# Kernel tuning notes

Measured on AMD Instinct MI355X. Metric: run time of the kernel, lower is better.

The kernel has to match this reference:

```python
import jax, jax.numpy as jnp
import numpy as np
from jax import lax

B, T, N, HID = 4, 144, 256, 64
CH, NC = 9, 4  # chunk_size_short, num_chunks_short


def setup_inputs():
    key = jax.random.key(0)
    ks = jax.random.split(key, 30)
    r = lambda i, sh, s=0.05: jax.random.normal(ks[i], sh, jnp.float32) * s
    adj = (jax.random.uniform(ks[1], (N, N)) < 0.1).astype(jnp.float32)
    adj = adj.at[jnp.arange(N), jnp.arange(N)].set(1.0)  # self-loops
    return {
        "seg": jax.random.normal(ks[0], (B, T, N, N), jnp.float32),
        "adj": adj,
        "dist": jax.random.uniform(ks[2], (N, N), jnp.float32),
        "W_gat": r(3, (N, HID)),
        "a_src": r(4, (HID,)),
        "a_dst": r(5, (HID,)),
        "lstm_Wih": r(6, (4 * HID, HID)),
        "lstm_Whh": r(7, (4 * HID, HID)),
        "lstm_bih": r(8, (4 * HID,)),
        "lstm_bhh": r(9, (4 * HID,)),
        "attnL_W": r(10, (HID, HID)),
        "attnL_b": r(11, (HID,)),
        "attnL_v": r(12, (HID,)),
        "gru_Wih": r(13, (NC, 3 * HID, HID)),
        "gru_Whh": r(14, (NC, 3 * HID, HID)),
        "gru_bih": r(15, (NC, 3 * HID)),
        "gru_bhh": r(16, (NC, 3 * HID)),
        "attnS_W": r(17, (NC, HID, HID)),
        "attnS_b": r(18, (NC, HID)),
        "attnS_v": r(19, (NC, HID)),
        "lin1_W": r(20, (2 * HID, HID + HID * NC)),
        "lin1_b": r(21, (2 * HID,)),
        "lin2_W": r(22, (N * N, 2 * HID)),
        "lin2_b": r(23, (N * N,)),
        "conv_k": r(24, (1, 1, 3, 3)),
        "conv_b": r(25, (1,)),
    }


def gat_features(seg, adj, dist, W_gat, a_src, a_dst):
    # Batches the per-timestep GAT over the time axis (B,T folded together).
    Wh = jnp.einsum('btnf,fh->btnh', seg, W_gat)                     # (B,T,N,H)
    e = jax.nn.leaky_relu((Wh @ a_src)[..., :, None] + (Wh @ a_dst)[..., None, :], 0.2)
    e = e - dist                                                     # distance penalty on logits
    logits = jnp.where(adj > 0, e, -1e9)                             # mask non-edges
    attn = jax.nn.softmax(logits, axis=-1)                           # (B,T,N,N)
    Hn = jax.nn.elu(jnp.einsum('btij,btjh->btih', attn, Wh))         # (B,T,N,H)
    return Hn.mean(axis=2)                                           # (B,T,H) mean-pool over nodes


def lstm(x, Wih, Whh, bih, bhh):
    h0 = jnp.zeros((x.shape[0], Whh.shape[1]), x.dtype)
    def step(carry, xt):
        h, c = carry
        g = xt @ Wih.T + bih + h @ Whh.T + bhh
        i, f, gg, o = jnp.split(g, 4, axis=-1)  # torch gate order i,f,g,o
        c = jax.nn.sigmoid(f) * c + jax.nn.sigmoid(i) * jnp.tanh(gg)
        h = jax.nn.sigmoid(o) * jnp.tanh(c)
        return (h, c), h
    _, ys = lax.scan(step, (h0, h0), jnp.swapaxes(x, 0, 1))
    return jnp.swapaxes(ys, 0, 1)


def gru(x, Wih, Whh, bih, bhh):
    h0 = jnp.zeros((x.shape[0], Whh.shape[1]), x.dtype)
    def step(h, xt):
        gx = xt @ Wih.T + bih
        gh = h @ Whh.T + bhh
        xr, xz, xn = jnp.split(gx, 3, axis=-1)  # torch gate order r,z,n
        hr, hz, hn = jnp.split(gh, 3, axis=-1)
        rr = jax.nn.sigmoid(xr + hr)
        zz = jax.nn.sigmoid(xz + hz)
        nn_ = jnp.tanh(xn + rr * hn)
        h = (1.0 - zz) * nn_ + zz * h
        return h, h
    _, ys = lax.scan(step, h0, jnp.swapaxes(x, 0, 1))
    return jnp.swapaxes(ys, 0, 1)


def tattn(h, W, b, v):
    s = jnp.tanh(h @ W + b) @ v          # (B,T) additive attention scores
    a = jax.nn.softmax(s, axis=1)
    return jnp.einsum('bt,bth->bh', a, h)


def reference(seg, adj, dist, W_gat, a_src, a_dst, lstm_Wih, lstm_Whh, lstm_bih, lstm_bhh,
              attnL_W, attnL_b, attnL_v, gru_Wih, gru_Whh, gru_bih, gru_bhh,
              attnS_W, attnS_b, attnS_v, lin1_W, lin1_b, lin2_W, lin2_b, conv_k, conv_b):
    Bsz = seg.shape[0]
    feats = gat_features(seg, adj, dist, W_gat, a_src, a_dst)        # (B,T,H)
    ctxL = tattn(lstm(feats, lstm_Wih, lstm_Whh, lstm_bih, lstm_bhh), attnL_W, attnL_b, attnL_v)
    # Short-term GCN features are the same GAT outputs on the last W_short steps.
    short = feats[:, -CH * NC:, :].reshape(Bsz, NC, CH, HID)
    gru_out = jax.vmap(gru, in_axes=(1, 0, 0, 0, 0), out_axes=1)(short, gru_Wih, gru_Whh, gru_bih, gru_bhh)
    ctxS = jax.vmap(tattn, in_axes=(1, 0, 0, 0), out_axes=1)(gru_out, attnS_W, attnS_b, attnS_v)  # (B,NC,H)
    fused = jnp.concatenate([ctxL, ctxS.reshape(Bsz, NC * HID)], axis=1)  # (B, 5H)
    h1 = jax.nn.relu(fused @ lin1_W.T + lin1_b)
    out = (h1 @ lin2_W.T + lin2_b).reshape(Bsz, 1, N, N)
    out = lax.conv_general_dilated(out, conv_k, (1, 1), 'SAME',
                                   dimension_numbers=('NCHW', 'OIHW', 'NCHW'))
    out = out + conv_b[None, :, None, None]
    return jax.nn.softplus(out[:, 0])
```

## Files before the change

### kernel.cpp

```cpp
#include <hip/hip_runtime.h>
#include <hip/hip_bf16.h>
#include <cstddef>


typedef __attribute__((ext_vector_type(8))) short bf16x8;
typedef __attribute__((ext_vector_type(4))) short bf16x4;
typedef __attribute__((ext_vector_type(4))) float f32x4;

__device__ __forceinline__ float sigf(float x) { return 1.0f / (1.0f + __expf(-x)); }
__device__ __forceinline__ float tanh_(float x) {
    x = fminf(fmaxf(x, -15.f), 15.f);
    float e = __expf(2.f * x);
    return (e - 1.f) / (e + 1.f);
}
__device__ __forceinline__ unsigned short f2b(float f) {
    unsigned u = __float_as_uint(f);
    u += 0x7FFFu + ((u >> 16) & 1u);
    return (unsigned short)(u >> 16);
}

__global__ void k_prep(const float* __restrict__ adj, const float* __restrict__ dist,
                       const float* __restrict__ W_gat,
                       float* __restrict__ M, unsigned short* __restrict__ Wt) {
    int blk = blockIdx.x, tid = threadIdx.x;
    if (blk < 256) {
        int i = blk * 256 + tid;
        M[i] = (adj[i] > 0.f) ? -dist[i] : -1e9f;
    } else {
        for (int it = 0; it < 64; ++it) {
            int e = it * 256 + tid;
            int k = e >> 6, c = e & 63;
            Wt[c * 256 + k] = f2b(W_gat[e]);
        }
    }
}

__global__ __launch_bounds__(256, 2) void k_gat(
    const float* __restrict__ seg, const unsigned short* __restrict__ Wt,
    const float* __restrict__ a_src, const float* __restrict__ a_dst,
    const float* __restrict__ Mmask, float* __restrict__ feats,
    const float* __restrict__ lWih, const float* __restrict__ lbih,
    const float* __restrict__ lbhh, float* __restrict__ gx) {
    __shared__ __align__(16) short A_s[256 * 64];
    __shared__ __align__(16) short Wt_s[64 * 64];
    __shared__ __align__(16) short WhT_s[64 * 256];
    __shared__ __align__(16) float svec[256];
    __shared__ __align__(16) float dvec[256];
    __shared__ __align__(16) float rmax[256];
    __shared__ __align__(16) float red[256];
    __shared__ __align__(16) float feats_l[64];

    const int tid  = threadIdx.x;
    const int lane = tid & 63;
    const int wv   = tid >> 6;
    const int wrow = wv * 64;
    const int bt   = blockIdx.x;
    const float* __restrict__ segp = seg + (size_t)bt * 65536;

    f32x4 acc[4][4];
    #pragma unroll
    for (int a = 0; a < 4; ++a)
        #pragma unroll
        for (int b = 0; b < 4; ++b) acc[a][b] = (f32x4)(0.f);

    for (int kc = 0; kc < 4; ++kc) {
        #pragma unroll
        for (int it = 0; it < 8; ++it) {
            int unit = it * 256 + tid;
            int row = unit >> 3, u = unit & 7;
            const float* g = segp + row * 256 + kc * 64 + u * 8;
            f32x4 v0 = *(const f32x4*)g;
            f32x4 v1 = *(const f32x4*)(g + 4);
            bf16x8 pk;
            pk[0] = (short)f2b(v0[0]); pk[1] = (short)f2b(v0[1]);
            pk[2] = (short)f2b(v0[2]); pk[3] = (short)f2b(v0[3]);
            pk[4] = (short)f2b(v1[0]); pk[5] = (short)f2b(v1[1]);
            pk[6] = (short)f2b(v1[2]); pk[7] = (short)f2b(v1[3]);
            *(bf16x8*)&A_s[(row * 8 + (u ^ (row & 7))) * 8] = pk;
        }
        #pragma unroll
        for (int it = 0; it < 2; ++it) {
            int unit = it * 256 + tid;
            int c = unit >> 3, u = unit & 7;
            bf16x8 w = *(const bf16x8*)(Wt + c * 256 + kc * 64 + u * 8);
            *(bf16x8*)&Wt_s[(c * 8 + (u ^ (c & 7))) * 8] = w;
        }
        __syncthreads();
        #pragma unroll
        for (int kt2 = 0; kt2 < 2; ++kt2) {
            int ku = kt2 * 4 + (lane >> 4);
            bf16x8 bfr[4];
            #pragma unroll
            for (int nt = 0; nt < 4; ++nt) {
                int col = nt * 16 + (lane & 15);
                bfr[nt] = *(const bf16x8*)&Wt_s[(col * 8 + (ku ^ (col & 7))) * 8];
            }
            #pragma unroll
            for (int mt = 0; mt < 4; ++mt) {
                int row = wrow + mt * 16 + (lane & 15);
                bf16x8 afr = *(const bf16x8*)&A_s[(row * 8 + (ku ^ (row & 7))) * 8];
                #pragma unroll
                for (int nt = 0; nt < 4; ++nt)
                    acc[mt][nt] = __builtin_amdgcn_mfma_f32_16x16x32_bf16(afr, bfr[nt], acc[mt][nt], 0, 0, 0);
            }
        }
        __syncthreads();
    }

    float asv[4], adv[4];
    #pragma unroll
    for (int nt = 0; nt < 4; ++nt) {
        asv[nt] = a_src[nt * 16 + (lane & 15)];
        adv[nt] = a_dst[nt * 16 + (lane & 15)];
    }
    #pragma unroll
    for (int mt = 0; mt < 4; ++mt) {
        #pragma unroll
        for (int r = 0; r < 4; ++r) {
            float ps = acc[mt][0][r] * asv[0] + acc[mt][1][r] * asv[1]
                     + acc[mt][2][r] * asv[2] + acc[mt][3][r] * asv[3];
            float pd = acc[mt][0][r] * adv[0] + acc[mt][1][r] * adv[1]
                     + acc[mt][2][r] * adv[2] + acc[mt][3][r] * adv[3];
            #pragma unroll
            for (int m = 1; m < 16; m <<= 1) {
                ps += __shfl_xor(ps, m);
                pd += __shfl_xor(pd, m);
            }
            if ((lane & 15) == 0) {
                int row = wrow + mt * 16 + (lane >> 4) * 4 + r;
                svec[row] = ps;
                dvec[row] = pd;
            }
        }
        #pragma unroll
        for (int nt = 0; nt < 4; ++nt) {
            int col  = nt * 16 + (lane & 15);
            int row0 = wrow + mt * 16 + (lane >> 4) * 4;
            bf16x4 pk4;
            pk4[0] = (short)f2b(acc[mt][nt][0]); pk4[1] = (short)f2b(acc[mt][nt][1]);
            pk4[2] = (short)f2b(acc[mt][nt][2]); pk4[3] = (short)f2b(acc[mt][nt][3]);
            int addr16 = col * 32 + ((row0 >> 3) ^ (col & 7));
            *(bf16x4*)&WhT_s[addr16 * 8 + (row0 & 7)] = pk4;
        }
    }
    __syncthreads();

    {
        float s_i = svec[tid];
        float m = -3.0e38f;
        const float* Mrow = Mmask + tid * 256;
        #pragma unroll 4
        for (int j4 = 0; j4 < 64; ++j4) {
            f32x4 mv = *(const f32x4*)(Mrow + j4 * 4);
            f32x4 dv = *(const f32x4*)&dvec[j4 * 4];
            #pragma unroll
            for (int e = 0; e < 4; ++e) {
                float x = s_i + dv[e];
                x = (x > 0.f) ? x : 0.2f * x;
                x += mv[e];
                m = fmaxf(m, x);
            }
        }
        rmax[tid] = m;
    }
    __syncthreads();

    f32x4 acc2[4][4];
    #pragma unroll
    for (int a = 0; a < 4; ++a)
        #pragma unroll
        for (int b = 0; b < 4; ++b) acc2[a][b] = (f32x4)(0.f);
    float psum[4] = {0.f, 0.f, 0.f, 0.f};
    float sv4[4], mx4[4];
    #pragma unroll
    for (int mt = 0; mt < 4; ++mt) {
        int row = wrow + mt * 16 + (lane & 15);
        sv4[mt] = svec[row];
        mx4[mt] = rmax[row];
    }
    const int jbase = (lane >> 4) * 8;
    #pragma unroll 1
    for (int kt = 0; kt < 8; ++kt) {
        int j0 = kt * 32 + jbase;
        int ku = kt * 4 + (lane >> 4);
        bf16x8 bfr[4];
        #pragma unroll
        for (int nt = 0; nt < 4; ++nt) {
            int col = nt * 16 + (lane & 15);
            bfr[nt] = *(const bf16x8*)&WhT_s[(col * 32 + (ku ^ (col & 7))) * 8];
        }
        f32x4 dv0 = *(const f32x4*)&dvec[j0];
        f32x4 dv1 = *(const f32x4*)&dvec[j0 + 4];
        #pragma unroll
        for (int mt = 0; mt < 4; ++mt) {
            int row = wrow + mt * 16 + (lane & 15);
            const float* Mp = Mmask + row * 256 + j0;
            f32x4 m0 = *(const f32x4*)Mp;
            f32x4 m1 = *(const f32x4*)(Mp + 4);
            float p[8];
            #pragma unroll
            for (int e = 0; e < 4; ++e) {
                float x = sv4[mt] + dv0[e];
                x = (x > 0.f) ? x : 0.2f * x;
                p[e] = __expf(x + m0[e] - mx4[mt]);
                float y = sv4[mt] + dv1[e];
                y = (y > 0.f) ? y : 0.2f * y;
                p[4 + e] = __expf(y + m1[e] - mx4[mt]);
            }
            psum[mt] += ((p[0] + p[1]) + (p[2] + p[3])) + ((p[4] + p[5]) + (p[6] + p[7]));
            bf16x8 pf;
            pf[0] = (short)f2b(p[0]); pf[1] = (short)f2b(p[1]);
            pf[2] = (short)f2b(p[2]); pf[3] = (short)f2b(p[3]);
            pf[4] = (short)f2b(p[4]); pf[5] = (short)f2b(p[5]);
            pf[6] = (short)f2b(p[6]); pf[7] = (short)f2b(p[7]);
            #pragma unroll
            for (int nt = 0; nt < 4; ++nt)
                acc2[mt][nt] = __builtin_amdgcn_mfma_f32_16x16x32_bf16(pf, bfr[nt], acc2[mt][nt], 0, 0, 0);
        }
    }
    #pragma unroll
    for (int mt = 0; mt < 4; ++mt) {
        psum[mt] += __shfl_xor(psum[mt], 16);
        psum[mt] += __shfl_xor(psum[mt], 32);
    }

    float part[4] = {0.f, 0.f, 0.f, 0.f};
    #pragma unroll
    for (int mt = 0; mt < 4; ++mt) {
        #pragma unroll
        for (int r = 0; r < 4; ++r) {
            float rs  = __shfl(psum[mt], ((lane >> 4) << 2) + r);
            float inv = 1.0f / rs;
            #pragma unroll
            for (int nt = 0; nt < 4; ++nt) {
                float x = acc2[mt][nt][r] * inv;
                x = (x > 0.f) ? x : expm1f(x);
                part[nt] += x;
            }
        }
    }
    #pragma unroll
    for (int nt = 0; nt < 4; ++nt) {
        part[nt] += __shfl_xor(part[nt], 16);
        part[nt] += __shfl_xor(part[nt], 32);
    }
    if ((lane >> 4) == 0) {
        #pragma unroll
        for (int nt = 0; nt < 4; ++nt) red[wv * 64 + nt * 16 + lane] = part[nt];
    }
    __syncthreads();
    if (tid < 64) {
        float f = (red[tid] + red[64 + tid] + red[128 + tid] + red[192 + tid]) * (1.0f / 256.0f);
        feats[bt * 64 + tid] = f;
        feats_l[tid] = f;
    }
    __syncthreads();

    {
        float a = lbih[tid] + lbhh[tid];
        const float* wp = lWih + tid * 64;
        #pragma unroll
        for (int k4 = 0; k4 < 16; ++k4) {
            f32x4 w = *(const f32x4*)(wp + k4 * 4);
            f32x4 x = *(const f32x4*)&feats_l[k4 * 4];
            a += w[0] * x[0] + w[1] * x[1] + w[2] * x[2] + w[3] * x[3];
        }
        gx[bt * 256 + tid] = a;
    }
}

__global__ __launch_bounds__(256) void k_rnn(
    const float* __restrict__ gx, const float* __restrict__ lWhh, float* __restrict__ lout,
    const float* __restrict__ feats, const float* __restrict__ gWih,
    const float* __restrict__ gWhh, const float* __restrict__ gbih,
    const float* __restrict__ gbhh, float* __restrict__ gout) {
    int tid = threadIdx.x;
    if (blockIdx.x < 4) {
        int b = blockIdx.x;
        int lane = tid & 63, wv = tid >> 6;
        __shared__ __align__(16) float hv[4][64];
        __shared__ __align__(16) float gl[2][256];
        float wr[64];
        #pragma unroll
        for (int q = 0; q < 16; ++q)
            *(f32x4*)&wr[q * 4] = *(const f32x4*)&lWhh[tid * 64 + q * 4];
        float c_s = 0.f;
        hv[wv][lane] = 0.f;
        for (int t = 0; t < 144; ++t) {
            float a = gx[(b * 144 + t) * 256 + tid];
            #pragma unroll
            for (int q = 0; q < 16; ++q) {
                f32x4 h4 = *(const f32x4*)&hv[wv][q * 4];
                a += wr[q * 4 + 0] * h4[0] + wr[q * 4 + 1] * h4[1]
                   + wr[q * 4 + 2] * h4[2] + wr[q * 4 + 3] * h4[3];
            }
            gl[t & 1][tid] = a;
            __syncthreads();
            float ig = gl[t & 1][lane],       fg = gl[t & 1][64 + lane],
                  gg = gl[t & 1][128 + lane], og = gl[t & 1][192 + lane];
            c_s = sigf(fg) * c_s + sigf(ig) * tanh_(gg);
            float h = sigf(og) * tanh_(c_s);
            hv[wv][lane] = h;
            if (wv == 0) lout[(b * 144 + t) * 64 + lane] = h;
        }
    } else {
        int bi_ = blockIdx.x - 4;
        int b = bi_ >> 2, c2 = bi_ & 3;
        __shared__ float hvg[64], xvg[64], gxl[192], ghl[192];
        float wi[64], wh[64], bi = 0.f, bh = 0.f, h_s = 0.f;
        if (tid < 192) {
            #pragma unroll
            for (int q = 0; q < 16; ++q) {
                *(f32x4*)&wi[q * 4] = *(const f32x4*)&gWih[(size_t)(c2 * 192 + tid) * 64 + q * 4];
                *(f32x4*)&wh[q * 4] = *(const f32x4*)&gWhh[(size_t)(c2 * 192 + tid) * 64 + q * 4];
            }
            bi = gbih[c2 * 192 + tid];
            bh = gbhh[c2 * 192 + tid];
        }
        if (tid < 64) hvg[tid] = 0.f;
        __syncthreads();
        for (int s = 0; s < 9; ++s) {
            int t = 108 + c2 * 9 + s;
            if (tid < 64) xvg[tid] = feats[(b * 144 + t) * 64 + tid];
            __syncthreads();
            if (tid < 192) {
                float ax = bi, ah = bh;
                #pragma unroll
                for (int k = 0; k < 64; ++k) { ax += wi[k] * xvg[k]; ah += wh[k] * hvg[k]; }
                gxl[tid] = ax; ghl[tid] = ah;
            }
            __syncthreads();
            if (tid < 64) {
                float xr = gxl[tid], xz = gxl[64 + tid], xn = gxl[128 + tid];
                float hr = ghl[tid], hz = ghl[64 + tid], hn = ghl[128 + tid];
                float rr = sigf(xr + hr), zz = sigf(xz + hz);
                float nn = tanh_(xn + rr * hn);
                h_s = (1.f - zz) * nn + zz * h_s;
                hvg[tid] = h_s;
                gout[((b * 4 + c2) * 9 + s) * 64 + tid] = h_s;
            }
            __syncthreads();
        }
    }
}

__global__ __launch_bounds__(256) void k_ctx(
    const float* __restrict__ lout, const float* __restrict__ aLW,
    const float* __restrict__ aLb, const float* __restrict__ aLv,
    const float* __restrict__ gout, const float* __restrict__ aSW,
    const float* __restrict__ aSb, const float* __restrict__ aSv,
    float* __restrict__ ctxL, float* __restrict__ ctxS) {
    int tid = threadIdx.x;
    if (blockIdx.x < 4) {
        int b = blockIdx.x;
        int tt = tid >> 6, hh = tid & 63;
        __shared__ __align__(16) float hbuf[4][64];
        __shared__ float sc[144];
        __shared__ float al[144];
        float wcol[64];
        #pragma unroll
        for (int k = 0; k < 64; ++k) wcol[k] = aLW[k * 64 + hh];
        float bb = aLb[hh], vv = aLv[hh];
        for (int g = 0; g < 36; ++g) {
            int t = g * 4 + tt;
            hbuf[tt][hh] = lout[(b * 144 + t) * 64 + hh];
            __syncthreads();
            float acc = bb;
            #pragma unroll
            for (int q = 0; q < 16; ++q) {
                f32x4 h4 = *(const f32x4*)&hbuf[tt][q * 4];
                acc += wcol[q * 4 + 0] * h4[0] + wcol[q * 4 + 1] * h4[1]
                     + wcol[q * 4 + 2] * h4[2] + wcol[q * 4 + 3] * h4[3];
            }
            float p = tanh_(acc) * vv;
            #pragma unroll
            for (int m = 1; m < 64; m <<= 1) p += __shfl_xor(p, m);
            if (hh == 0) sc[t] = p;
            __syncthreads();
        }
        float mx = -3e38f;
        for (int t2 = 0; t2 < 144; ++t2) mx = fmaxf(mx, sc[t2]);
        float ss = 0.f;
        for (int t2 = 0; t2 < 144; ++t2) ss += __expf(sc[t2] - mx);
        float inv = 1.f / ss;
        if (tid < 144) al[tid] = __expf(sc[tid] - mx) * inv;
        __syncthreads();
        if (tid < 64) {
            float acc = 0.f;
            for (int t2 = 0; t2 < 144; ++t2) acc += al[t2] * lout[(b * 144 + t2) * 64 + tid];
            ctxL[b * 64 + tid] = acc;
        }
    } else {
        int bi_ = blockIdx.x - 4;
        int b = bi_ >> 2, c2 = bi_ & 3;
        __shared__ float xv2[64];
        if (tid < 64) {
            int lane = tid;
            const float* Wc = aSW + c2 * 4096;
            float wcol[64];
            #pragma unroll
            for (int k = 0; k < 64; ++k) wcol[k] = Wc[k * 64 + lane];
            float bb = aSb[c2 * 64 + lane], vv = aSv[c2 * 64 + lane];
            float sv[9], hl[9];
            #pragma unroll 1
            for (int s = 0; s < 9; ++s) {
                float h = gout[((size_t)((b * 4 + c2) * 9 + s)) * 64 + lane];
                hl[s] = h;
                xv2[lane] = h;
                float acc = bb;
                #pragma unroll
                for (int k = 0; k < 64; ++k) acc += wcol[k] * xv2[k];
                float p = tanh_(acc) * vv;
                #pragma unroll
                for (int m = 1; m < 64; m <<= 1) p += __shfl_xor(p, m);
                sv[s] = p;
            }
            float mx = -3e38f;
            #pragma unroll
            for (int s = 0; s < 9; ++s) mx = fmaxf(mx, sv[s]);
            float ss = 0.f;
            #pragma unroll
            for (int s = 0; s < 9; ++s) { sv[s] = __expf(sv[s] - mx); ss += sv[s]; }
            float inv = 1.f / ss;
            float acc = 0.f;
            #pragma unroll
            for (int s = 0; s < 9; ++s) acc += sv[s] * inv * hl[s];
            ctxS[(b * 4 + c2) * 64 + lane] = acc;
        }
    }
}

__global__ __launch_bounds__(512) void k_lin1(
    const float* __restrict__ ctxL, const float* __restrict__ ctxS,
    const float* __restrict__ W, const float* __restrict__ bb,
    float* __restrict__ h1) {
    int tid = threadIdx.x;
    __shared__ __align__(16) float fu[4 * 320];
    for (int c = tid; c < 1280; c += 512) {
        int b2 = c / 320, k = c % 320;
        fu[c] = (k < 64) ? ctxL[b2 * 64 + k] : ctxS[b2 * 256 + (k - 64)];
    }
    __syncthreads();
    int b = tid >> 7, r = tid & 127;
    float acc = bb[r];
    #pragma unroll 4
    for (int k4 = 0; k4 < 80; ++k4) {
        f32x4 w = *(const f32x4*)&W[r * 320 + k4 * 4];
        f32x4 x = *(const f32x4*)&fu[b * 320 + k4 * 4];
        acc += w[0] * x[0] + w[1] * x[1] + w[2] * x[2] + w[3] * x[3];
    }
    h1[b * 128 + r] = fmaxf(acc, 0.f);
}

__global__ __launch_bounds__(256) void k_lin2(
    const float* __restrict__ h1, const float* __restrict__ W,
    const float* __restrict__ bb, float* __restrict__ h2) {
    int tid = threadIdx.x, blk = blockIdx.x;
    __shared__ __align__(16) float Wc[256 * 33];
    __shared__ __align__(16) float h1l[512];
    for (int c = tid; c < 512; c += 256) h1l[c] = h1[c];
    int r = blk * 256 + tid;
    float a0, a1, a2, a3;
    a0 = a1 = a2 = a3 = bb[r];
    for (int kc = 0; kc < 4; ++kc) {
        __syncthreads();
        for (int it = 0; it < 32; ++it) {
            int c = it * 256 + tid;
            int row = c >> 5, kk = c & 31;
            Wc[row * 33 + kk] = W[(size_t)(blk * 256 + row) * 128 + kc * 32 + kk];
        }
        __syncthreads();
        #pragma unroll
        for (int kk = 0; kk < 32; ++kk) {
            float w = Wc[tid * 33 + kk];
            a0 += w * h1l[kc * 32 + kk];
            a1 += w * h1l[128 + kc * 32 + kk];
            a2 += w * h1l[256 + kc * 32 + kk];
            a3 += w * h1l[384 + kc * 32 + kk];
        }
    }
    h2[r] = a0;
    h2[65536 + r] = a1;
    h2[2 * 65536 + r] = a2;
    h2[3 * 65536 + r] = a3;
}

__global__ __launch_bounds__(256) void k_conv(
    const float* __restrict__ h2, const float* __restrict__ ck,
    const float* __restrict__ cb, float* __restrict__ out) {
    int x = threadIdx.x;
    int b = blockIdx.x >> 8, y = blockIdx.x & 255;
    float kk[9];
    #pragma unroll
    for (int i = 0; i < 9; ++i) kk[i] = ck[i];
    const float* base = h2 + b * 65536;
    float acc = cb[0];
    #pragma unroll
    for (int dy = -1; dy <= 1; ++dy) {
        int yy = y + dy;
        if (yy < 0 || yy > 255) continue;
        #pragma unroll
        for (int dx = -1; dx <= 1; ++dx) {
            int xx = x + dx;
            if (xx < 0 || xx > 255) continue;
            acc += base[yy * 256 + xx] * kk[(dy + 1) * 3 + (dx + 1)];
        }
    }
    float r = (acc > 20.f) ? acc : log1pf(__expf(acc));
    out[b * 65536 + y * 256 + x] = r;
}

extern "C" void kernel_launch(void* const* d_in, const int* in_sizes, int n_in,
                              void* d_out, int out_size, void* d_ws, size_t ws_size,
                              hipStream_t stream) {
    const float* seg   = (const float*)d_in[0];
    const float* adj   = (const float*)d_in[1];
    const float* dist  = (const float*)d_in[2];
    const float* W_gat = (const float*)d_in[3];
    const float* a_src = (const float*)d_in[4];
    const float* a_dst = (const float*)d_in[5];
    const float* lWih  = (const float*)d_in[6];
    const float* lWhh  = (const float*)d_in[7];
    const float* lbih  = (const float*)d_in[8];
    const float* lbhh  = (const float*)d_in[9];
    const float* aLW   = (const float*)d_in[10];
    const float* aLb   = (const float*)d_in[11];
    const float* aLv   = (const float*)d_in[12];
    const float* gWih  = (const float*)d_in[13];
    const float* gWhh  = (const float*)d_in[14];
    const float* gbih  = (const float*)d_in[15];
    const float* gbhh  = (const float*)d_in[16];
    const float* aSW   = (const float*)d_in[17];
    const float* aSb   = (const float*)d_in[18];
    const float* aSv   = (const float*)d_in[19];
    const float* l1W   = (const float*)d_in[20];
    const float* l1b   = (const float*)d_in[21];
    const float* l2W   = (const float*)d_in[22];
    const float* l2b   = (const float*)d_in[23];
    const float* ck    = (const float*)d_in[24];
    const float* cb    = (const float*)d_in[25];
    float* out = (float*)d_out;

    float* ws    = (float*)d_ws;
    float* M     = ws;
    float* feats = M + 65536;
    float* gx    = feats + 36864;
    float* lout  = gx + 147456;
    float* ctxL  = lout + 36864;
    float* gout  = ctxL + 256;
    float* ctxS  = gout + 9216;
    float* h1    = ctxS + 1024;
    float* h2    = h1 + 512;
    unsigned short* Wt = (unsigned short*)(h2 + 262144 - 8192);

    k_prep<<<257, 256, 0, stream>>>(adj, dist, W_gat, M, Wt);
    k_gat<<<576, 256, 0, stream>>>(seg, Wt, a_src, a_dst, M, feats, lWih, lbih, lbhh, gx);
    k_rnn<<<20, 256, 0, stream>>>(gx, lWhh, lout, feats, gWih, gWhh, gbih, gbhh, gout);
    k_ctx<<<20, 256, 0, stream>>>(lout, aLW, aLb, aLv, gout, aSW, aSb, aSv, ctxL, ctxS);
    k_lin1<<<1, 512, 0, stream>>>(ctxL, ctxS, l1W, l1b, h1);
    k_lin2<<<256, 256, 0, stream>>>(h1, l2W, l2b, h2);
    k_conv<<<1024, 256, 0, stream>>>(h2, ck, cb, out);
}
```

Baseline: 271.6 us.

## Shrink GAT shared memory, bf16 mask, global softmax bound, retile lin2 and ctx

Stores the additive mask as bf16 to halve its reads, and loads W_gat fragments straight from global memory so the seg tile and the Wh transpose can share one LDS buffer. This lets occupancy go from 2 to 3 blocks. The per-row softmax max pass is replaced by one block-wide upper bound, max(s)+max(d) through leaky-relu, which removes a full pass over the mask. The risk is underflow for rows whose own logits sit far below that bound, and the mask loses precision in bf16. It also adds packed bf16 conversion, a restructured lin2 over 512 blocks with vectorised weight loads and a split-K reduction, and caches lout in LDS inside k_ctx.

```diff
diff --git a/kernel.cpp b/kernel.cpp
--- a/kernel.cpp
+++ b/kernel.cpp
@@ -4,7 +4,6 @@
 
 
 typedef __attribute__((ext_vector_type(8))) short bf16x8;
-typedef __attribute__((ext_vector_type(4))) short bf16x4;
 typedef __attribute__((ext_vector_type(4))) float f32x4;
 
 __device__ __forceinline__ float sigf(float x) { return 1.0f / (1.0f + __expf(-x)); }
@@ -18,14 +17,21 @@
     u += 0x7FFFu + ((u >> 16) & 1u);
     return (unsigned short)(u >> 16);
 }
+__device__ __forceinline__ unsigned pk2(float lo, float hi) {
+    __hip_bfloat162 h = __float22bfloat162_rn(float2{lo, hi});
+    return *reinterpret_cast<unsigned*>(&h);
+}
+__device__ __forceinline__ float b2f(short s) {
+    return __uint_as_float(((unsigned)(unsigned short)s) << 16);
+}
 
 __global__ void k_prep(const float* __restrict__ adj, const float* __restrict__ dist,
                        const float* __restrict__ W_gat,
-                       float* __restrict__ M, unsigned short* __restrict__ Wt) {
+                       unsigned short* __restrict__ Mb, unsigned short* __restrict__ Wt) {
     int blk = blockIdx.x, tid = threadIdx.x;
     if (blk < 256) {
         int i = blk * 256 + tid;
-        M[i] = (adj[i] > 0.f) ? -dist[i] : -1e9f;
+        Mb[i] = f2b((adj[i] > 0.f) ? -dist[i] : -1e9f);
     } else {
         for (int it = 0; it < 64; ++it) {
             int e = it * 256 + tid;
@@ -35,18 +41,15 @@
     }
 }
 
-__global__ __launch_bounds__(256, 2) void k_gat(
+__global__ __launch_bounds__(256, 3) void k_gat(
     const float* __restrict__ seg, const unsigned short* __restrict__ Wt,
     const float* __restrict__ a_src, const float* __restrict__ a_dst,
-    const float* __restrict__ Mmask, float* __restrict__ feats,
+    const unsigned short* __restrict__ Mb, float* __restrict__ feats,
     const float* __restrict__ lWih, const float* __restrict__ lbih,
     const float* __restrict__ lbhh, float* __restrict__ gx) {
-    __shared__ __align__(16) short A_s[256 * 64];
-    __shared__ __align__(16) short Wt_s[64 * 64];
-    __shared__ __align__(16) short WhT_s[64 * 256];
+    __shared__ __align__(16) short AB_s[256 * 64];
     __shared__ __align__(16) float svec[256];
     __shared__ __align__(16) float dvec[256];
-    __shared__ __align__(16) float rmax[256];
     __shared__ __align__(16) float red[256];
     __shared__ __align__(16) float feats_l[64];
 
@@ -71,37 +74,32 @@
             const float* g = segp + row * 256 + kc * 64 + u * 8;
             f32x4 v0 = *(const f32x4*)g;
             f32x4 v1 = *(const f32x4*)(g + 4);
-            bf16x8 pk;
-            pk[0] = (short)f2b(v0[0]); pk[1] = (short)f2b(v0[1]);
-            pk[2] = (short)f2b(v0[2]); pk[3] = (short)f2b(v0[3]);
-            pk[4] = (short)f2b(v1[0]); pk[5] = (short)f2b(v1[1]);
-            pk[6] = (short)f2b(v1[2]); pk[7] = (short)f2b(v1[3]);
-            *(bf16x8*)&A_s[(row * 8 + (u ^ (row & 7))) * 8] = pk;
-        }
-        #pragma unroll
-        for (int it = 0; it < 2; ++it) {
-            int unit = it * 256 + tid;
-            int c = unit >> 3, u = unit & 7;
-            bf16x8 w = *(const bf16x8*)(Wt + c * 256 + kc * 64 + u * 8);
-            *(bf16x8*)&Wt_s[(c * 8 + (u ^ (c & 7))) * 8] = w;
-        }
-        __syncthreads();
+            uint4 pk;
+            pk.x = pk2(v0[0], v0[1]); pk.y = pk2(v0[2], v0[3]);
+            pk.z = pk2(v1[0], v1[1]); pk.w = pk2(v1[2], v1[3]);
+            *(uint4*)&AB_s[(row * 8 + (u ^ (row & 7))) * 8] = pk;
+        }
+        bf16x8 bfr[2][4];
         #pragma unroll
         for (int kt2 = 0; kt2 < 2; ++kt2) {
             int ku = kt2 * 4 + (lane >> 4);
-            bf16x8 bfr[4];
             #pragma unroll
             for (int nt = 0; nt < 4; ++nt) {
                 int col = nt * 16 + (lane & 15);
-                bfr[nt] = *(const bf16x8*)&Wt_s[(col * 8 + (ku ^ (col & 7))) * 8];
-            }
+                bfr[kt2][nt] = *(const bf16x8*)(Wt + col * 256 + kc * 64 + ku * 8);
+            }
+        }
+        __syncthreads();
+        #pragma unroll
+        for (int kt2 = 0; kt2 < 2; ++kt2) {
+            int ku = kt2 * 4 + (lane >> 4);
             #pragma unroll
             for (int mt = 0; mt < 4; ++mt) {
                 int row = wrow + mt * 16 + (lane & 15);
-                bf16x8 afr = *(const bf16x8*)&A_s[(row * 8 + (ku ^ (row & 7))) * 8];
+                bf16x8 afr = *(const bf16x8*)&AB_s[(row * 8 + (ku ^ (row & 7))) * 8];
                 #pragma unroll
                 for (int nt = 0; nt < 4; ++nt)
-                    acc[mt][nt] = __builtin_amdgcn_mfma_f32_16x16x32_bf16(afr, bfr[nt], acc[mt][nt], 0, 0, 0);
+                    acc[mt][nt] = __builtin_amdgcn_mfma_f32_16x16x32_bf16(afr, bfr[kt2][nt], acc[mt][nt], 0, 0, 0);
             }
         }
         __syncthreads();
@@ -136,34 +134,32 @@
         for (int nt = 0; nt < 4; ++nt) {
             int col  = nt * 16 + (lane & 15);
             int row0 = wrow + mt * 16 + (lane >> 4) * 4;
-            bf16x4 pk4;
-            pk4[0] = (short)f2b(acc[mt][nt][0]); pk4[1] = (short)f2b(acc[mt][nt][1]);
-            pk4[2] = (short)f2b(acc[mt][nt][2]); pk4[3] = (short)f2b(acc[mt][nt][3]);
+            uint2 pk4;
+            pk4.x = pk2(acc[mt][nt][0], acc[mt][nt][1]);
+            pk4.y = pk2(acc[mt][nt][2], acc[mt][nt][3]);
             int addr16 = col * 32 + ((row0 >> 3) ^ (col & 7));
-            *(bf16x4*)&WhT_s[addr16 * 8 + (row0 & 7)] = pk4;
+            *(uint2*)&AB_s[addr16 * 8 + (row0 & 7)] = pk4;
         }
     }
     __syncthreads();
 
     {
-        float s_i = svec[tid];
-        float m = -3.0e38f;
-        const float* Mrow = Mmask + tid * 256;
-        #pragma unroll 4
-        for (int j4 = 0; j4 < 64; ++j4) {
-            f32x4 mv = *(const f32x4*)(Mrow + j4 * 4);
-            f32x4 dv = *(const f32x4*)&dvec[j4 * 4];
-            #pragma unroll
-            for (int e = 0; e < 4; ++e) {
-                float x = s_i + dv[e];
-                x = (x > 0.f) ? x : 0.2f * x;
-                x += mv[e];
-                m = fmaxf(m, x);
-            }
-        }
-        rmax[tid] = m;
-    }
-    __syncthreads();
+        float a = svec[tid], b = dvec[tid];
+        #pragma unroll
+        for (int m = 1; m < 64; m <<= 1) {
+            a = fmaxf(a, __shfl_xor(a, m));
+            b = fmaxf(b, __shfl_xor(b, m));
+        }
+        if (lane == 0) { red[wv] = a; red[4 + wv] = b; }
+    }
+    __syncthreads();
+    float mB;
+    {
+        float ms = fmaxf(fmaxf(red[0], red[1]), fmaxf(red[2], red[3]));
+        float md = fmaxf(fmaxf(red[4], red[5]), fmaxf(red[6], red[7]));
+        float x = ms + md;
+        mB = fmaxf(x, 0.2f * x);
+    }
 
     f32x4 acc2[4][4];
     #pragma unroll
@@ -171,51 +167,44 @@
         #pragma unroll
         for (int b = 0; b < 4; ++b) acc2[a][b] = (f32x4)(0.f);
     float psum[4] = {0.f, 0.f, 0.f, 0.f};
-    float sv4[4], mx4[4];
-    #pragma unroll
-    for (int mt = 0; mt < 4; ++mt) {
-        int row = wrow + mt * 16 + (lane & 15);
-        sv4[mt] = svec[row];
-        mx4[mt] = rmax[row];
-    }
+    float sv4[4];
+    #pragma unroll
+    for (int mt = 0; mt < 4; ++mt) sv4[mt] = svec[wrow + mt * 16 + (lane & 15)];
     const int jbase = (lane >> 4) * 8;
     #pragma unroll 1
     for (int kt = 0; kt < 8; ++kt) {
         int j0 = kt * 32 + jbase;
         int ku = kt * 4 + (lane >> 4);
-        bf16x8 bfr[4];
+        bf16x8 bfr2[4];
         #pragma unroll
         for (int nt = 0; nt < 4; ++nt) {
             int col = nt * 16 + (lane & 15);
-            bfr[nt] = *(const bf16x8*)&WhT_s[(col * 32 + (ku ^ (col & 7))) * 8];
+            bfr2[nt] = *(const bf16x8*)&AB_s[(col * 32 + (ku ^ (col & 7))) * 8];
         }
         f32x4 dv0 = *(const f32x4*)&dvec[j0];
         f32x4 dv1 = *(const f32x4*)&dvec[j0 + 4];
         #pragma unroll
         for (int mt = 0; mt < 4; ++mt) {
             int row = wrow + mt * 16 + (lane & 15);
-            const float* Mp = Mmask + row * 256 + j0;
-            f32x4 m0 = *(const f32x4*)Mp;
-            f32x4 m1 = *(const f32x4*)(Mp + 4);
+            bf16x8 mrow = *(const bf16x8*)(Mb + row * 256 + j0);
             float p[8];
             #pragma unroll
             for (int e = 0; e < 4; ++e) {
-                float x = sv4[mt] + dv0[e];
-                x = (x > 0.f) ? x : 0.2f * x;
-                p[e] = __expf(x + m0[e] - mx4[mt]);
-                float y = sv4[mt] + dv1[e];
-                y = (y > 0.f) ? y : 0.2f * y;
-                p[4 + e] = __expf(y + m1[e] - mx4[mt]);
+                float u = sv4[mt] + dv0[e];
+                u = fmaxf(u, 0.2f * u);
+                p[e] = __expf(u + b2f(mrow[e]) - mB);
+                float w = sv4[mt] + dv1[e];
+                w = fmaxf(w, 0.2f * w);
+                p[4 + e] = __expf(w + b2f(mrow[4 + e]) - mB);
             }
             psum[mt] += ((p[0] + p[1]) + (p[2] + p[3])) + ((p[4] + p[5]) + (p[6] + p[7]));
-            bf16x8 pf;
-            pf[0] = (short)f2b(p[0]); pf[1] = (short)f2b(p[1]);
-            pf[2] = (short)f2b(p[2]); pf[3] = (short)f2b(p[3]);
-            pf[4] = (short)f2b(p[4]); pf[5] = (short)f2b(p[5]);
-            pf[6] = (short)f2b(p[6]); pf[7] = (short)f2b(p[7]);
+            uint4 upf;
+            upf.x = pk2(p[0], p[1]); upf.y = pk2(p[2], p[3]);
+            upf.z = pk2(p[4], p[5]); upf.w = pk2(p[6], p[7]);
+            bf16x8 pf = *reinterpret_cast<bf16x8*>(&upf);
             #pragma unroll
             for (int nt = 0; nt < 4; ++nt)
-                acc2[mt][nt] = __builtin_amdgcn_mfma_f32_16x16x32_bf16(pf, bfr[nt], acc2[mt][nt], 0, 0, 0);
+                acc2[mt][nt] = __builtin_amdgcn_mfma_f32_16x16x32_bf16(pf, bfr2[nt], acc2[mt][nt], 0, 0, 0);
         }
     }
     #pragma unroll
@@ -353,31 +342,31 @@
     int tid = threadIdx.x;
     if (blockIdx.x < 4) {
         int b = blockIdx.x;
-        int tt = tid >> 6, hh = tid & 63;
-        __shared__ __align__(16) float hbuf[4][64];
+        int wv = tid >> 6, lane = tid & 63;
+        __shared__ __align__(16) float Hl[144 * 64];
         __shared__ float sc[144];
         __shared__ float al[144];
+        for (int i = tid; i < 9216; i += 256) Hl[i] = lout[b * 9216 + i];
         float wcol[64];
         #pragma unroll
-        for (int k = 0; k < 64; ++k) wcol[k] = aLW[k * 64 + hh];
-        float bb = aLb[hh], vv = aLv[hh];
+        for (int k = 0; k < 64; ++k) wcol[k] = aLW[k * 64 + lane];
+        float bb = aLb[lane], vv = aLv[lane];
+        __syncthreads();
         for (int g = 0; g < 36; ++g) {
-            int t = g * 4 + tt;
-            hbuf[tt][hh] = lout[(b * 144 + t) * 64 + hh];
-            __syncthreads();
+            int t = g * 4 + wv;
             float acc = bb;
             #pragma unroll
             for (int q = 0; q < 16; ++q) {
-                f32x4 h4 = *(const f32x4*)&hbuf[tt][q * 4];
+                f32x4 h4 = *(const f32x4*)&Hl[t * 64 + q * 4];
                 acc += wcol[q * 4 + 0] * h4[0] + wcol[q * 4 + 1] * h4[1]
                      + wcol[q * 4 + 2] * h4[2] + wcol[q * 4 + 3] * h4[3];
             }
             float p = tanh_(acc) * vv;
             #pragma unroll
             for (int m = 1; m < 64; m <<= 1) p += __shfl_xor(p, m);
-            if (hh == 0) sc[t] = p;
-            __syncthreads();
-        }
+            if (lane == 0) sc[t] = p;
+        }
+        __syncthreads();
         float mx = -3e38f;
         for (int t2 = 0; t2 < 144; ++t2) mx = fmaxf(mx, sc[t2]);
         float ss = 0.f;
@@ -387,7 +376,7 @@
         __syncthreads();
         if (tid < 64) {
             float acc = 0.f;
-            for (int t2 = 0; t2 < 144; ++t2) acc += al[t2] * lout[(b * 144 + t2) * 64 + tid];
+            for (int t2 = 0; t2 < 144; ++t2) acc += al[t2] * Hl[t2 * 64 + tid];
             ctxL[b * 64 + tid] = acc;
         }
     } else {
@@ -456,33 +445,46 @@
     const float* __restrict__ h1, const float* __restrict__ W,
     const float* __restrict__ bb, float* __restrict__ h2) {
     int tid = threadIdx.x, blk = blockIdx.x;
-    __shared__ __align__(16) float Wc[256 * 33];
+    __shared__ __align__(16) float Wc[128 * 132];
     __shared__ __align__(16) float h1l[512];
+    __shared__ __align__(16) float red2[512];
     for (int c = tid; c < 512; c += 256) h1l[c] = h1[c];
-    int r = blk * 256 + tid;
-    float a0, a1, a2, a3;
-    a0 = a1 = a2 = a3 = bb[r];
-    for (int kc = 0; kc < 4; ++kc) {
-        __syncthreads();
-        for (int it = 0; it < 32; ++it) {
-            int c = it * 256 + tid;
-            int row = c >> 5, kk = c & 31;
-            Wc[row * 33 + kk] = W[(size_t)(blk * 256 + row) * 128 + kc * 32 + kk];
-        }
-        __syncthreads();
-        #pragma unroll
-        for (int kk = 0; kk < 32; ++kk) {
-            float w = Wc[tid * 33 + kk];
-            a0 += w * h1l[kc * 32 + kk];
-            a1 += w * h1l[128 + kc * 32 + kk];
-            a2 += w * h1l[256 + kc * 32 + kk];
-            a3 += w * h1l[384 + kc * 32 + kk];
-        }
-    }
-    h2[r] = a0;
-    h2[65536 + r] = a1;
-    h2[2 * 65536 + r] = a2;
-    h2[3 * 65536 + r] = a3;
+    #pragma unroll
+    for (int it = 0; it < 16; ++it) {
+        int flat = it * 1024 + tid * 4;
+        int row = flat >> 7, col = flat & 127;
+        f32x4 v = *(const f32x4*)&W[(size_t)(blk * 128 + row) * 128 + col];
+        *(f32x4*)&Wc[row * 132 + col] = v;
+    }
+    __syncthreads();
+    int r2 = tid >> 1, half = tid & 1;
+    float a0 = 0.f, a1 = 0.f, a2 = 0.f, a3 = 0.f;
+    #pragma unroll
+    for (int i = 0; i < 16; ++i) {
+        f32x4 w = *(const f32x4*)&Wc[r2 * 132 + half * 64 + i * 4];
+        f32x4 x0 = *(const f32x4*)&h1l[half * 64 + i * 4];
+        f32x4 x1 = *(const f32x4*)&h1l[128 + half * 64 + i * 4];
+        f32x4 x2 = *(const f32x4*)&h1l[256 + half * 64 + i * 4];
+        f32x4 x3 = *(const f32x4*)&h1l[384 + half * 64 + i * 4];
+        a0 += w[0] * x0[0] + w[1] * x0[1] + w[2] * x0[2] + w[3] * x0[3];
+        a1 += w[0] * x1[0] + w[1] * x1[1] + w[2] * x1[2] + w[3] * x1[3];
+        a2 += w[0] * x2[0] + w[1] * x2[1] + w[2] * x2[2] + w[3] * x2[3];
+        a3 += w[0] * x3[0] + w[1] * x3[1] + w[2] * x3[2] + w[3] * x3[3];
+    }
+    if (half == 1) {
+        f32x4 v; v[0] = a0; v[1] = a1; v[2] = a2; v[3] = a3;
+        *(f32x4*)&red2[r2 * 4] = v;
+    }
+    __syncthreads();
+    if (half == 0) {
+        f32x4 v = *(const f32x4*)&red2[r2 * 4];
+        int r = blk * 128 + r2;
+        float bv = bb[r];
+        h2[r]              = a0 + v[0] + bv;
+        h2[65536 + r]      = a1 + v[1] + bv;
+        h2[2 * 65536 + r]  = a2 + v[2] + bv;
+        h2[3 * 65536 + r]  = a3 + v[3] + bv;
+    }
 }
 
 __global__ __launch_bounds__(256) void k_conv(
@@ -542,8 +544,8 @@
     float* out = (float*)d_out;
 
     float* ws    = (float*)d_ws;
-    float* M     = ws;
-    float* feats = M + 65536;
+    unsigned short* Mb = (unsigned short*)ws;
+    float* feats = ws + 32768;
     float* gx    = feats + 36864;
     float* lout  = gx + 147456;
     float* ctxL  = lout + 36864;
@@ -551,13 +553,13 @@
     float* ctxS  = gout + 9216;
     float* h1    = ctxS + 1024;
     float* h2    = h1 + 512;
-    unsigned short* Wt = (unsigned short*)(h2 + 262144 - 8192);
-
-    k_prep<<<257, 256, 0, stream>>>(adj, dist, W_gat, M, Wt);
-    k_gat<<<576, 256, 0, stream>>>(seg, Wt, a_src, a_dst, M, feats, lWih, lbih, lbhh, gx);
+    unsigned short* Wt = (unsigned short*)(h2 + 262144);
+
+    k_prep<<<257, 256, 0, stream>>>(adj, dist, W_gat, Mb, Wt);
+    k_gat<<<576, 256, 0, stream>>>(seg, Wt, a_src, a_dst, Mb, feats, lWih, lbih, lbhh, gx);
     k_rnn<<<20, 256, 0, stream>>>(gx, lWhh, lout, feats, gWih, gWhh, gbih, gbhh, gout);
     k_ctx<<<20, 256, 0, stream>>>(lout, aLW, aLb, aLv, gout, aSW, aSb, aSv, ctxL, ctxS);
     k_lin1<<<1, 512, 0, stream>>>(ctxL, ctxS, l1W, l1b, h1);
-    k_lin2<<<256, 256, 0, stream>>>(h1, l2W, l2b, h2);
+    k_lin2<<<512, 256, 0, stream>>>(h1, l2W, l2b, h2);
     k_conv<<<1024, 256, 0, stream>>>(h2, ck, cb, out);
 }
```

Result: faster. 236.2 us (-13.0%).
